# Optimization experiments

Hardware: AMD Instinct MI355X
Metric: run time of the kernel (lower is better)

Reference implementation:

```python
import jax, jax.numpy as jnp
import numpy as np
from jax import lax

K_NEIGHBORS = 15
LAM = 1.0
EPS = 1e-8


def _cdist(a):
    # Euclidean pairwise distance, safe sqrt (zero diag has zero grad path handled in bwd module too)
    sq = jnp.sum(a * a, axis=1)
    d2 = sq[:, None] + sq[None, :] - 2.0 * (a @ a.T)
    d2 = jnp.maximum(d2, 0.0)
    safe = jnp.where(d2 > 0.0, d2, 1.0)
    return jnp.where(d2 > 0.0, jnp.sqrt(safe), 0.0)


def _knn_loss(z, x, k):
    B = x.shape[0]
    x_dist = _cdist(x)
    z_dist = _cdist(z)
    eye = jnp.eye(B, dtype=bool)
    x_ns = jnp.where(eye, jnp.inf, x_dist)  # fill_diagonal_(inf)
    _, knn_idx = lax.top_k(-x_ns, k)        # k smallest per row
    mask = jnp.zeros((B, B), dtype=bool).at[jnp.arange(B)[:, None], knn_idx].set(True)
    mask = mask | mask.T
    x_max = jnp.max(jnp.where(mask, x_dist, -jnp.inf))
    z_max = jnp.max(jnp.where(mask, z_dist, -jnp.inf))
    x_norm = x_dist / (x_max + EPS)
    z_norm = z_dist / (z_max + EPS)
    diff2 = (z_norm - x_norm) ** 2
    # mean over masked entries == masked_select(...).mean()
    return jnp.sum(jnp.where(mask, diff2, 0.0)) / jnp.sum(mask).astype(diff2.dtype)


def setup_inputs() -> dict:
    key = jax.random.key(0)
    ks = jax.random.split(key, 13)
    D, H1, H2, L = 1024, 2048, 512, 64

    def lin(k, fan_in, fan_out):
        bound = 1.0 / np.sqrt(fan_in)
        kw, kb = jax.random.split(k)
        w = jax.random.uniform(kw, (fan_in, fan_out), jnp.float32, -bound, bound)
        b = jax.random.uniform(kb, (fan_out,), jnp.float32, -bound, bound)
        return w, b

    x = jax.random.normal(ks[0], (8192, D), jnp.float32)
    w_e0, b_e0 = lin(ks[1], D, H1)
    w_e1, b_e1 = lin(ks[2], H1, H2)
    w_e2, b_e2 = lin(ks[3], H2, L)
    w_d0, b_d0 = lin(ks[4], L, H2)
    w_d1, b_d1 = lin(ks[5], H2, H1)
    w_d2, b_d2 = lin(ks[6], H1, D)
    return {"x": x,
            "w_e0": w_e0, "b_e0": b_e0, "w_e1": w_e1, "b_e1": b_e1, "w_e2": w_e2, "b_e2": b_e2,
            "w_d0": w_d0, "b_d0": b_d0, "w_d1": w_d1, "b_d1": b_d1, "w_d2": w_d2, "b_d2": b_d2}


def reference(x, w_e0, b_e0, w_e1, b_e1, w_e2, b_e2, w_d0, b_d0, w_d1, b_d1, w_d2, b_d2):
    h = jax.nn.relu(x @ w_e0 + b_e0)
    h = jax.nn.relu(h @ w_e1 + b_e1)
    z = h @ w_e2 + b_e2
    h = jax.nn.relu(z @ w_d0 + b_d0)
    h = jax.nn.relu(h @ w_d1 + b_d1)
    x_rec = h @ w_d2 + b_d2
    rec_loss = jnp.mean((x_rec - x) ** 2)
    knn_loss = _knn_loss(z, x, K_NEIGHBORS)
    total = rec_loss + LAM * knn_loss
    return (total, z, rec_loss, knn_loss)
```

## Files before the change

kernel.cpp:

```cpp
#include <hip/hip_runtime.h>


typedef __attribute__((ext_vector_type(8))) short bf16x8;
typedef __attribute__((ext_vector_type(4))) float f32x4;

#define DEVINL static __device__ __forceinline__

DEVINL unsigned short f2bf(float f){
  unsigned u = __float_as_uint(f);
  u += 0x7FFFu + ((u >> 16) & 1u);
  return (unsigned short)(u >> 16);
}

DEVINL int med3i(int a, int b, int c){
  int d;
  asm("v_med3_i32 %0, %1, %2, %3" : "=v"(d) : "v"(a), "v"(b), "v"(c));
  return d;
}

DEVINL void gload16(const unsigned short* g, void* lds){
  __builtin_amdgcn_global_load_lds(
      (const __attribute__((address_space(1))) unsigned int*)g,
      (__attribute__((address_space(3))) unsigned int*)lds, 16, 0, 0);
}

DEVINL void lds_barrier(){
  asm volatile("s_waitcnt lgkmcnt(0)" ::: "memory");
  __builtin_amdgcn_s_barrier();
  asm volatile("" ::: "memory");
}

#define NLISTS 39

#define INS15(NAME, R0,R1,R2,R3,R4,R5,R6,R7,R8,R9,R10,R11,R12,R13,R14)  \
  auto NAME = [&](int v){                                               \
    if (v < R14){                                                       \
      R14 = med3i(v, R13, R14); R13 = med3i(v, R12, R13);               \
      R12 = med3i(v, R11, R12); R11 = med3i(v, R10, R11);               \
      R10 = med3i(v, R9 , R10); R9  = med3i(v, R8 , R9 );               \
      R8  = med3i(v, R7 , R8 ); R7  = med3i(v, R6 , R7 );               \
      R6  = med3i(v, R5 , R6 ); R5  = med3i(v, R4 , R5 );               \
      R4  = med3i(v, R3 , R4 ); R3  = med3i(v, R2 , R3 );               \
      R2  = med3i(v, R1 , R2 ); R1  = med3i(v, R0 , R1 );               \
      R0  = min(R0, v);                                                 \
    }                                                                   \
  }

__global__ __launch_bounds__(256) void cvtT_k(const float* __restrict__ x,
    unsigned short* __restrict__ xb, float* __restrict__ xsq,
    const float* __restrict__ w0, const float* __restrict__ w1,
    const float* __restrict__ w2, const float* __restrict__ w3,
    const float* __restrict__ w4, const float* __restrict__ w5,
    unsigned short* __restrict__ t0, unsigned short* __restrict__ t1,
    unsigned short* __restrict__ t2, unsigned short* __restrict__ t3,
    unsigned short* __restrict__ t4, unsigned short* __restrict__ t5)
{
  __shared__ float t[32][33];
  const int tid = threadIdx.x;
  if (blockIdx.x >= 2048){
    int id = blockIdx.x - 2048;
    const float* w; unsigned short* wt; int K, N, loc;
    if      (id < 2048){ w = w0; wt = t0; K = 1024; N = 2048; loc = id; }
    else if (id < 3072){ w = w1; wt = t1; K = 2048; N = 512;  loc = id - 2048; }
    else if (id < 3104){ w = w2; wt = t2; K = 512;  N = 64;   loc = id - 3072; }
    else if (id < 3136){ w = w3; wt = t3; K = 64;   N = 512;  loc = id - 3104; }
    else if (id < 4160){ w = w4; wt = t4; K = 512;  N = 2048; loc = id - 3136; }
    else               { w = w5; wt = t5; K = 2048; N = 1024; loc = id - 4160; }
    const int ntn = N >> 5;
    const int n0 = (loc % ntn) << 5, k0 = (loc / ntn) << 5;
    const int tx = tid & 31, ty = tid >> 5;
    #pragma unroll
    for (int q = 0; q < 4; q++)
      t[ty + 8*q][tx] = w[(size_t)(k0 + ty + 8*q) * N + n0 + tx];
    __syncthreads();
    #pragma unroll
    for (int q = 0; q < 4; q++)
      wt[(size_t)(n0 + ty + 8*q) * K + k0 + tx] = f2bf(t[tx][ty + 8*q]);
    return;
  }
  const int lane = tid & 63, wv = tid >> 6;
  const int row = blockIdx.x * 4 + wv;
  const float4* px = (const float4*)(x + (size_t)row * 1024);
  ushort4* pb = (ushort4*)(xb + (size_t)row * 1024);
  float ss = 0.f;
  #pragma unroll
  for (int q = 0; q < 4; q++){
    float4 v = px[q * 64 + lane];
    ss += v.x*v.x + v.y*v.y + v.z*v.z + v.w*v.w;
    ushort4 o; o.x = f2bf(v.x); o.y = f2bf(v.y); o.z = f2bf(v.z); o.w = f2bf(v.w);
    pb[q * 64 + lane] = o;
  }
  #pragma unroll
  for (int o = 32; o; o >>= 1) ss += __shfl_xor(ss, o);
  if (!lane) xsq[row] = ss;
}

__global__ __launch_bounds__(256, 2) void thr_k(
    const unsigned short* __restrict__ Xb, const float* __restrict__ xsq,
    int* __restrict__ thrI)
{
  __shared__ short As[128][32];
  __shared__ unsigned short d2s[128][130];
  const int tid = threadIdx.x, lane = tid & 63, wid = tid >> 6;
  const int wr = wid >> 1, wc = wid & 1;
  const int r16 = lane & 15, kg = lane >> 4;
  const int srow = lane >> 2, scol = (lane & 3) * 8;
  const float INF = __builtin_inff();
  const int b0 = blockIdx.x * 128;

  float xr[4][4];
  #pragma unroll
  for (int m = 0; m < 4; m++)
    #pragma unroll
    for (int r = 0; r < 4; r++)
      xr[m][r] = xsq[b0 + wr*64 + m*16 + kg*4 + r];

  const unsigned short* pa = Xb + (size_t)(b0 + wid*16 + srow) * 1024 + scol;
  short* ldsA0 = &As[wid*16][0];
  short* ldsA1 = &As[wid*16 + 64][0];

  f32x4 acc[4][4] = {};
  for (int k0 = 0; k0 < 1024; k0 += 32){
    __syncthreads();
    gload16(pa, ldsA0);
    gload16(pa + 65536, ldsA1);
    pa += 32;
    __syncthreads();
    bf16x8 af[4], bfr[4];
    #pragma unroll
    for (int m = 0; m < 4; m++) af[m]  = *(const bf16x8*)&As[wr*64 + m*16 + r16][kg*8];
    #pragma unroll
    for (int n = 0; n < 4; n++) bfr[n] = *(const bf16x8*)&As[wc*64 + n*16 + r16][kg*8];
    #pragma unroll
    for (int m = 0; m < 4; m++)
      #pragma unroll
      for (int n = 0; n < 4; n++)
        acc[m][n] = __builtin_amdgcn_mfma_f32_16x16x32_bf16(af[m], bfr[n], acc[m][n], 0, 0, 0);
  }
  float xc[4];
  #pragma unroll
  for (int n = 0; n < 4; n++) xc[n] = xsq[b0 + wc*64 + n*16 + r16];
  #pragma unroll
  for (int m = 0; m < 4; m++){
    #pragma unroll
    for (int n = 0; n < 4; n++){
      const int lc = wc*64 + n*16 + r16;
      #pragma unroll
      for (int r = 0; r < 4; r++){
        const int lr = wr*64 + m*16 + kg*4 + r;
        float v = xr[m][r] + xc[n] - 2.f * acc[m][n][r];
        if (lr == lc) v = INF;
        d2s[lr][lc] = f2bf(v);
      }
    }
  }
  __syncthreads();
  if (tid < 128){
    int r0,r1,r2,r3,r4,r5,r6,r7,r8,r9,r10,r11,r12,r13,r14;
    r0=r1=r2=r3=r4=r5=r6=r7=r8=r9=r10=r11=r12=r13=r14=0x7FFFFFFF;
    INS15(ins, r0,r1,r2,r3,r4,r5,r6,r7,r8,r9,r10,r11,r12,r13,r14);
    #pragma unroll 4
    for (int cc = 0; cc < 128; cc += 2){
      unsigned pv = *(const unsigned*)&d2s[tid][cc];
      ins((int)((pv << 16) | (unsigned)cc));
      ins((int)((pv & 0xFFFF0000u) | (unsigned)(cc + 1)));
    }
    thrI[b0 + tid] = (int)(((unsigned)r14 & 0xFFFF0000u) | 0xFFFFu);
  }
}

template<int BM, int BN, int WM, int WN, bool RELU, int OMODE>
__global__ __launch_bounds__(256, 2) void gemm_bt(
    const unsigned short* __restrict__ A, const unsigned short* __restrict__ Bt,
    const float* __restrict__ bias, int M, int N, int K,
    unsigned short* __restrict__ Cb, float* __restrict__ Cf,
    const float* __restrict__ Xref, float* __restrict__ recPart)
{
  constexpr int FM = BM / (WM * 16), FN = BN / (WN * 16);
  constexpr int AIT = (BM/16 + 3) / 4, BIT = (BN/16 + 3) / 4;
  __shared__ short As[BM][32];
  __shared__ short Bs[BN][32];
  __shared__ float wsum[4];
  const int tid = threadIdx.x, lane = tid & 63, wid = tid >> 6;
  const int wr = wid / WN, wc = wid % WN;
  const int r16 = lane & 15, kg = lane >> 4;
  const int row0 = blockIdx.x * BM, col0 = blockIdx.y * BN;
  const int srow = lane >> 2, scol = (lane & 3) * 8;
  (void)M;
  const size_t chS = (size_t)64 * K;
  const unsigned short* pa = A  + (size_t)(row0 + wid*16 + srow) * K + scol;
  const unsigned short* pb = Bt + (size_t)(col0 + wid*16 + srow) * K + scol;
  f32x4 acc[FM][FN] = {};
  for (int k0 = 0; k0 < K; k0 += 32){
    __syncthreads();
    #pragma unroll
    for (int it = 0; it < AIT; ++it)
      if (it*4 + wid < BM/16)
        gload16(pa + it*chS, &As[(it*4 + wid)*16][0]);
    #pragma unroll
    for (int it = 0; it < BIT; ++it)
      if (it*4 + wid < BN/16)
        gload16(pb + it*chS, &Bs[(it*4 + wid)*16][0]);
    pa += 32; pb += 32;
    __syncthreads();
    bf16x8 af[FM], bfr[FN];
    #pragma unroll
    for (int m = 0; m < FM; m++) af[m]  = *(const bf16x8*)&As[wr*FM*16 + m*16 + r16][kg*8];
    #pragma unroll
    for (int n = 0; n < FN; n++) bfr[n] = *(const bf16x8*)&Bs[wc*FN*16 + n*16 + r16][kg*8];
    #pragma unroll
    for (int m = 0; m < FM; m++)
      #pragma unroll
      for (int n = 0; n < FN; n++)
        acc[m][n] = __builtin_amdgcn_mfma_f32_16x16x32_bf16(af[m], bfr[n], acc[m][n], 0, 0, 0);
  }
  float lsum = 0.f;
  #pragma unroll
  for (int m = 0; m < FM; m++){
    #pragma unroll
    for (int n = 0; n < FN; n++){
      const int gc = col0 + wc*FN*16 + n*16 + r16;
      const float bv = bias[gc];
      #pragma unroll
      for (int r = 0; r < 4; r++){
        const int gr = row0 + wr*FM*16 + m*16 + kg*4 + r;
        float v = acc[m][n][r] + bv;
        if (RELU) v = fmaxf(v, 0.f);
        if (OMODE == 2){
          float d = v - Xref[(size_t)gr * N + gc];
          lsum += d * d;
        } else {
          Cb[(size_t)gr * N + gc] = f2bf(v);
          if (OMODE == 1) Cf[(size_t)gr * N + gc] = v;
        }
      }
    }
  }
  if (OMODE == 2){
    #pragma unroll
    for (int o = 32; o; o >>= 1) lsum += __shfl_xor(lsum, o);
    if (!lane) wsum[wid] = lsum;
    __syncthreads();
    if (!tid) recPart[blockIdx.y * gridDim.x + blockIdx.x] =
        wsum[0] + wsum[1] + wsum[2] + wsum[3];
  }
}

__global__ __launch_bounds__(256, 2) void gram_topk_k(
    const unsigned short* __restrict__ Xb, const float* __restrict__ xsq,
    const int* __restrict__ thrI, int* __restrict__ topP,
    const unsigned short* __restrict__ gBt, const float* __restrict__ gBias,
    unsigned short* __restrict__ gC)
{
  __shared__ short As[128][32];
  __shared__ short Bs[128][32];
  __shared__ unsigned short d2s[128][130];
  __shared__ int colL[128][15];
  __shared__ unsigned bkt[16][256];
  const int tid = threadIdx.x, lane = tid & 63, wid = tid >> 6;
  const int wr = wid >> 1, wc = wid & 1;
  const int r16 = lane & 15, kg = lane >> 4;
  const int srow = lane >> 2, scol = (lane & 3) * 8;

  short* ldsA0 = &As[wid*16][0];  short* ldsA1 = &As[wid*16 + 64][0];
  short* ldsB0 = &Bs[wid*16][0];  short* ldsB1 = &Bs[wid*16 + 64][0];
  auto stage2 = [&](const unsigned short* pa, const unsigned short* pb){
    gload16(pa,         ldsA0);
    gload16(pa + 65536, ldsA1);
    gload16(pb,         ldsB0);
    gload16(pb + 65536, ldsB1);
  };

  if (blockIdx.x >= 512){
    const int gb = blockIdx.x - 512;
    const int row0 = (gb & 63) * 128, col0 = (gb >> 6) * 128;
    const unsigned short* pa = Xb  + (size_t)(row0 + wid*16 + srow) * 1024 + scol;
    const unsigned short* pb = gBt + (size_t)(col0 + wid*16 + srow) * 1024 + scol;
    f32x4 acc[4][4] = {};
    for (int k0 = 0; k0 < 1024; k0 += 32){
      __syncthreads();
      stage2(pa, pb);
      pa += 32; pb += 32;
      __syncthreads();
      bf16x8 af[4], bfr[4];
      #pragma unroll
      for (int m = 0; m < 4; m++) af[m]  = *(const bf16x8*)&As[wr*64 + m*16 + r16][kg*8];
      #pragma unroll
      for (int n = 0; n < 4; n++) bfr[n] = *(const bf16x8*)&Bs[wc*64 + n*16 + r16][kg*8];
      #pragma unroll
      for (int m = 0; m < 4; m++)
        #pragma unroll
        for (int n = 0; n < 4; n++)
          acc[m][n] = __builtin_amdgcn_mfma_f32_16x16x32_bf16(af[m], bfr[n], acc[m][n], 0, 0, 0);
    }
    #pragma unroll
    for (int m = 0; m < 4; m++){
      #pragma unroll
      for (int n = 0; n < 4; n++){
        const int gc = col0 + wc*64 + n*16 + r16;
        const float bv = gBias[gc];
        #pragma unroll
        for (int r = 0; r < 4; r++){
          const int gr = row0 + wr*64 + m*16 + kg*4 + r;
          gC[(size_t)gr * 2048 + gc] = f2bf(fmaxf(acc[m][n][r] + bv, 0.f));
        }
      }
    }
    return;
  }

  const float INF = __builtin_inff();
  const int INFI = 0x7FFFFFFF;
  const int bi = blockIdx.x & 63;
  const int cl = blockIdx.x >> 6;
  const int row0 = bi * 128;
  const int ntt = (cl == 7) ? 5 : 4;
  const int selrow = tid & 127, half = tid >> 7, selc0 = half * 64;
  const int thrRI = thrI[row0 + selrow];

  const unsigned short* aB = Xb + (size_t)(row0 + wid*16 + srow) * 1024 + scol;

  int r0,r1,r2,r3,r4,r5,r6,r7,r8,r9,r10,r11,r12,r13,r14;
  r0=r1=r2=r3=r4=r5=r6=r7=r8=r9=r10=r11=r12=r13=r14=INFI;
  INS15(insR, r0,r1,r2,r3,r4,r5,r6,r7,r8,r9,r10,r11,r12,r13,r14);
  int c0,c1,c2,c3,c4,c5,c6,c7,c8,c9,c10,c11,c12,c13,c14;
  INS15(insC, c0,c1,c2,c3,c4,c5,c6,c7,c8,c9,c10,c11,c12,c13,c14);

  float xr[4][4];
  #pragma unroll
  for (int m = 0; m < 4; m++)
    #pragma unroll
    for (int r = 0; r < 4; r++)
      xr[m][r] = xsq[row0 + wr*64 + m*16 + kg*4 + r];

  stage2(aB, Xb + (size_t)(((bi + cl*4) & 63) * 128 + wid*16 + srow) * 1024 + scol);

  for (int tt = 0; tt < ntt; ++tt){
    const int d = cl * 4 + tt;
    const int bj = (bi + d) & 63;
    const int j0 = bj * 128;
    const unsigned short* bB  = Xb + (size_t)(j0 + wid*16 + srow) * 1024 + scol;
    const unsigned short* bBn = Xb + (size_t)(((bi + d + 1) & 63) * 128 + wid*16 + srow) * 1024 + scol;
    const unsigned short* pa = aB;
    const unsigned short* pb = bB;
    f32x4 acc[4][4] = {};
    for (int k0 = 0; k0 < 1024; k0 += 32){
      __syncthreads();
      bf16x8 af[4], bfr[4];
      #pragma unroll
      for (int m = 0; m < 4; m++) af[m]  = *(const bf16x8*)&As[wr*64 + m*16 + r16][kg*8];
      #pragma unroll
      for (int n = 0; n < 4; n++) bfr[n] = *(const bf16x8*)&Bs[wc*64 + n*16 + r16][kg*8];
      __syncthreads();
      if (k0 + 32 < 1024){ pa += 32; pb += 32; stage2(pa, pb); }
      else if (tt + 1 < ntt) stage2(aB, bBn);
      #pragma unroll
      for (int m = 0; m < 4; m++)
        #pragma unroll
        for (int n = 0; n < 4; n++)
          acc[m][n] = __builtin_amdgcn_mfma_f32_16x16x32_bf16(af[m], bfr[n], acc[m][n], 0, 0, 0);
    }
    float xc[4];
    #pragma unroll
    for (int n = 0; n < 4; n++) xc[n] = xsq[j0 + wc*64 + n*16 + r16];
    #pragma unroll
    for (int m = 0; m < 4; m++){
      #pragma unroll
      for (int n = 0; n < 4; n++){
        const int lc = wc*64 + n*16 + r16;
        #pragma unroll
        for (int r = 0; r < 4; r++){
          const int lr = wr*64 + m*16 + kg*4 + r;
          float v = xr[m][r] + xc[n] - 2.f * acc[m][n][r];
          if (row0 + lr == j0 + lc) v = INF;
          d2s[lr][lc] = f2bf(v);
        }
      }
    }
    lds_barrier();

    {
      int cnt = 0;
      const int jg0 = j0 + selc0;
      #pragma unroll 4
      for (int cc = 0; cc < 64; cc += 2){
        unsigned pv = *(const unsigned*)&d2s[selrow][selc0 + cc];
        int p0 = (int)((pv << 16) | (unsigned)(jg0 + cc));
        int p1 = (int)((pv & 0xFFFF0000u) | (unsigned)(jg0 + cc + 1));
        if (p0 <= thrRI){
          if (cnt < 16){ bkt[cnt][tid] = (unsigned)p0; ++cnt; } else insR(p0);
        }
        if (p1 <= thrRI){
          if (cnt < 16){ bkt[cnt][tid] = (unsigned)p1; ++cnt; } else insR(p1);
        }
      }
      for (int q = 0; q < cnt; ++q) insR((int)bkt[q][tid]);
    }

    const bool doCol = (d >= 1) && (d <= 31);
    if (doCol){
      c0=c1=c2=c3=c4=c5=c6=c7=c8=c9=c10=c11=c12=c13=c14=INFI;
      const int thrCI = thrI[j0 + selrow];
      const int rbase = row0 + selc0;
      int cnt = 0;
      #pragma unroll 4
      for (int rr = 0; rr < 64; ++rr){
        unsigned v = d2s[selc0 + rr][selrow];
        int pk = (int)((v << 16) | (unsigned)(rbase + rr));
        if (pk <= thrCI){
          if (cnt < 16){ bkt[cnt][tid] = (unsigned)pk; ++cnt; } else insC(pk);
        }
      }
      for (int q = 0; q < cnt; ++q) insC((int)bkt[q][tid]);
      if (half){
        colL[selrow][0]=c0;  colL[selrow][1]=c1;  colL[selrow][2]=c2;
        colL[selrow][3]=c3;  colL[selrow][4]=c4;  colL[selrow][5]=c5;
        colL[selrow][6]=c6;  colL[selrow][7]=c7;  colL[selrow][8]=c8;
        colL[selrow][9]=c9;  colL[selrow][10]=c10; colL[selrow][11]=c11;
        colL[selrow][12]=c12; colL[selrow][13]=c13; colL[selrow][14]=c14;
      }
    }
    lds_barrier();
    if (doCol && !half){
      #pragma unroll 1
      for (int q = 0; q < 15; ++q){
        int v = colL[selrow][q];
        if (v >= c14) break;
        insC(v);
      }
      int* dst = topP + ((size_t)(j0 + selrow) * NLISTS + (8 + d - 1)) * 15;
      dst[0]=c0;  dst[1]=c1;  dst[2]=c2;  dst[3]=c3;  dst[4]=c4;
      dst[5]=c5;  dst[6]=c6;  dst[7]=c7;  dst[8]=c8;  dst[9]=c9;
      dst[10]=c10; dst[11]=c11; dst[12]=c12; dst[13]=c13; dst[14]=c14;
    }
  }
  lds_barrier();
  if (half){
    colL[selrow][0]=r0;  colL[selrow][1]=r1;  colL[selrow][2]=r2;
    colL[selrow][3]=r3;  colL[selrow][4]=r4;  colL[selrow][5]=r5;
    colL[selrow][6]=r6;  colL[selrow][7]=r7;  colL[selrow][8]=r8;
    colL[selrow][9]=r9;  colL[selrow][10]=r10; colL[selrow][11]=r11;
    colL[selrow][12]=r12; colL[selrow][13]=r13; colL[selrow][14]=r14;
  }
  lds_barrier();
  if (!half){
    #pragma unroll 1
    for (int q = 0; q < 15; ++q){
      int v = colL[selrow][q];
      if (v >= r14) break;
      insR(v);
    }
    int* dst = topP + ((size_t)(row0 + selrow) * NLISTS + cl) * 15;
    dst[0]=r0;  dst[1]=r1;  dst[2]=r2;  dst[3]=r3;  dst[4]=r4;
    dst[5]=r5;  dst[6]=r6;  dst[7]=r7;  dst[8]=r8;  dst[9]=r9;
    dst[10]=r10; dst[11]=r11; dst[12]=r12; dst[13]=r13; dst[14]=r14;
  }
}

__global__ __launch_bounds__(256) void merge_topk_k(const int* __restrict__ topP,
    int* __restrict__ knn, float* __restrict__ d2k, float* __restrict__ xpart)
{
  __shared__ float wmax[4];
  const int lane = threadIdx.x & 63, wid = threadIdx.x >> 6;
  const int row = blockIdx.x * 4 + wid;
  const int* tp = topP + (size_t)row * (NLISTS * 15);
  const int INFI = 0x7FFFFFFF;
  int c0 = tp[lane];
  int c1 = tp[lane + 64];
  int c2 = tp[lane + 128];
  int c3 = tp[lane + 192];
  int c4 = tp[lane + 256];
  int c5 = tp[lane + 320];
  int c6 = tp[lane + 384];
  int c7 = tp[lane + 448];
  int c8 = tp[lane + 512];
  int c9 = (lane < 9) ? tp[lane + 576] : INFI;
  float last = 0.f;
  for (int it = 0; it < 15; ++it){
    int m = min(min(min(c0, c1), min(c2, c3)), min(min(c4, c5), min(c6, c7)));
    m = min(m, min(c8, c9));
    #pragma unroll
    for (int o = 32; o; o >>= 1) m = min(m, __shfl_xor(m, o));
    if (!lane){
      knn[row * 15 + it] = m & 0xFFFF;
      float f = __uint_as_float((unsigned)m & 0xFFFF0000u);
      d2k[row * 15 + it] = f;
      last = f;
    }
    c0 = (c0 == m) ? INFI : c0;   c1 = (c1 == m) ? INFI : c1;
    c2 = (c2 == m) ? INFI : c2;   c3 = (c3 == m) ? INFI : c3;
    c4 = (c4 == m) ? INFI : c4;   c5 = (c5 == m) ? INFI : c5;
    c6 = (c6 == m) ? INFI : c6;   c7 = (c7 == m) ? INFI : c7;
    c8 = (c8 == m) ? INFI : c8;   c9 = (c9 == m) ? INFI : c9;
  }
  if (!lane) wmax[wid] = last;
  __syncthreads();
  if (!threadIdx.x)
    xpart[blockIdx.x] = fmaxf(fmaxf(wmax[0], wmax[1]), fmaxf(wmax[2], wmax[3]));
}

__global__ __launch_bounds__(256) void pair_sums_k(
    const float* __restrict__ z, const int* __restrict__ knn,
    const float* __restrict__ d2k,
    float* __restrict__ zzP, float* __restrict__ zxP, float* __restrict__ xxP,
    float* __restrict__ zmP, float* __restrict__ cntP)
{
  __shared__ float red[4][5];
  const int lane = threadIdx.x & 63, wid = threadIdx.x >> 6;
  float szz = 0.f, szx = 0.f, sxx = 0.f, mz = 0.f, scnt = 0.f;
  for (int p = blockIdx.x * 4 + wid; p < 122880; p += gridDim.x * 4){
    const int i = p / 15;
    const int j = knn[p];
    const float dx2 = d2k[p];
    float dd = z[(size_t)i * 64 + lane] - z[(size_t)j * 64 + lane];
    float s = dd * dd;
    #pragma unroll
    for (int o = 32; o; o >>= 1) s += __shfl_xor(s, o);
    int kj = knn[j * 15 + min(lane, 14)];
    unsigned long long m2 = __ballot(lane < 15 && kj == i);
    const float w = m2 ? 1.f : 2.f;
    float dz = sqrtf(s), dx = sqrtf(dx2);
    szz += w * s;
    szx += w * dz * dx;
    sxx += w * dx2;
    scnt += w;
    mz = fmaxf(mz, dz);
  }
  if (!lane){
    red[wid][0] = szz; red[wid][1] = szx; red[wid][2] = sxx;
    red[wid][3] = mz;  red[wid][4] = scnt;
  }
  __syncthreads();
  if (!threadIdx.x){
    float a = 0.f, b = 0.f, c = 0.f, m = 0.f, n = 0.f;
    #pragma unroll
    for (int w = 0; w < 4; w++){
      a += red[w][0]; b += red[w][1]; c += red[w][2];
      m = fmaxf(m, red[w][3]); n += red[w][4];
    }
    zzP[blockIdx.x] = a; zxP[blockIdx.x] = b; xxP[blockIdx.x] = c;
    zmP[blockIdx.x] = m; cntP[blockIdx.x] = n;
  }
}

__global__ __launch_bounds__(256) void final_reduce_k(
    const float* __restrict__ recPart, const float* __restrict__ xpart,
    const float* __restrict__ zzP, const float* __restrict__ zxP,
    const float* __restrict__ xxP, const float* __restrict__ zmP,
    const float* __restrict__ cntP, float* __restrict__ out)
{
  __shared__ float rd[4][7];
  const int t = threadIdx.x, lane = t & 63, wid = t >> 6;
  float rec = 0.f, xm = 0.f, zz = 0.f, zx = 0.f, xx = 0.f, zm = 0.f, cnt = 0.f;
  for (int i = t; i < 1024; i += 256) rec += recPart[i];
  for (int i = t; i < 2048; i += 256) xm = fmaxf(xm, xpart[i]);
  for (int i = t; i < 1920; i += 256){
    zz += zzP[i]; zx += zxP[i]; xx += xxP[i]; cnt += cntP[i];
    zm = fmaxf(zm, zmP[i]);
  }
  #pragma unroll
  for (int o = 32; o; o >>= 1){
    rec += __shfl_xor(rec, o); zz += __shfl_xor(zz, o);
    zx  += __shfl_xor(zx, o);  xx += __shfl_xor(xx, o);
    cnt += __shfl_xor(cnt, o);
    xm = fmaxf(xm, __shfl_xor(xm, o));
    zm = fmaxf(zm, __shfl_xor(zm, o));
  }
  if (!lane){
    rd[wid][0]=rec; rd[wid][1]=zz; rd[wid][2]=zx; rd[wid][3]=xx;
    rd[wid][4]=xm;  rd[wid][5]=zm; rd[wid][6]=cnt;
  }
  __syncthreads();
  if (!t){
    rec = rd[0][0]+rd[1][0]+rd[2][0]+rd[3][0];
    zz  = rd[0][1]+rd[1][1]+rd[2][1]+rd[3][1];
    zx  = rd[0][2]+rd[1][2]+rd[2][2]+rd[3][2];
    xx  = rd[0][3]+rd[1][3]+rd[2][3]+rd[3][3];
    xm  = fmaxf(fmaxf(rd[0][4],rd[1][4]), fmaxf(rd[2][4],rd[3][4]));
    zm  = fmaxf(fmaxf(rd[0][5],rd[1][5]), fmaxf(rd[2][5],rd[3][5]));
    cnt = rd[0][6]+rd[1][6]+rd[2][6]+rd[3][6];
    rec *= 1.0f / (8192.0f * 1024.0f);
    float xmax = sqrtf(xm);
    float rx = 1.0f / (xmax + 1e-8f), rz = 1.0f / (zm + 1e-8f);
    float knn = (zz * rz * rz - 2.0f * zx * rz * rx + xx * rx * rx) / cnt;
    out[0] = rec + knn;
    out[1 + 8192 * 64]     = rec;
    out[1 + 8192 * 64 + 1] = knn;
  }
}

extern "C" void kernel_launch(void* const* d_in, const int* in_sizes, int n_in,
                              void* d_out, int out_size, void* d_ws, size_t ws_size,
                              hipStream_t stream)
{
  (void)in_sizes; (void)n_in; (void)out_size;
  const float* x    = (const float*)d_in[0];
  const float* w_e0 = (const float*)d_in[1];  const float* b_e0 = (const float*)d_in[2];
  const float* w_e1 = (const float*)d_in[3];  const float* b_e1 = (const float*)d_in[4];
  const float* w_e2 = (const float*)d_in[5];  const float* b_e2 = (const float*)d_in[6];
  const float* w_d0 = (const float*)d_in[7];  const float* b_d0 = (const float*)d_in[8];
  const float* w_d1 = (const float*)d_in[9];  const float* b_d1 = (const float*)d_in[10];
  const float* w_d2 = (const float*)d_in[11]; const float* b_d2 = (const float*)d_in[12];
  float* out = (float*)d_out;

  char* ws = (char*)d_ws;
  size_t off = 0;
  auto alloc = [&](size_t bytes) -> void* {
    void* p = ws + off;
    off += (bytes + 255) & ~(size_t)255;
    return p;
  };
  unsigned short* xb   = (unsigned short*)alloc(8192ull * 1024 * 2);
  unsigned short* wte0 = (unsigned short*)alloc(2048ull * 1024 * 2);
  unsigned short* wte1 = (unsigned short*)alloc(512ull  * 2048 * 2);
  unsigned short* wte2 = (unsigned short*)alloc(64ull   * 512  * 2);
  unsigned short* wtd0 = (unsigned short*)alloc(512ull  * 64   * 2);
  unsigned short* wtd1 = (unsigned short*)alloc(2048ull * 512  * 2);
  unsigned short* wtd2 = (unsigned short*)alloc(1024ull * 2048 * 2);
  unsigned short* bufA = (unsigned short*)alloc(8192ull * 2048 * 2);
  unsigned short* bufB = (unsigned short*)alloc(8192ull * 512  * 2);
  unsigned short* zb   = (unsigned short*)alloc(8192ull * 64   * 2);
  int*   topP   = (int*)  alloc(8192ull * NLISTS * 15 * 4);
  float* xsq    = (float*)alloc(8192 * 4);
  int*   thrI   = (int*)  alloc(8192 * 4);
  int*   knn    = (int*)  alloc(8192ull * 15 * 4);
  float* d2k    = (float*)alloc(8192ull * 15 * 4);
  float* xpart  = (float*)alloc(2048 * 4);
  float* zzP    = (float*)alloc(1920 * 4);
  float* zxP    = (float*)alloc(1920 * 4);
  float* xxP    = (float*)alloc(1920 * 4);
  float* zmP    = (float*)alloc(1920 * 4);
  float* cntP   = (float*)alloc(1920 * 4);
  float* recPart= (float*)alloc(1024 * 4);
  if (off > ws_size) return;

  cvtT_k<<<8256, 256, 0, stream>>>(x, xb, xsq,
      w_e0, w_e1, w_e2, w_d0, w_d1, w_d2, wte0, wte1, wte2, wtd0, wtd1, wtd2);

  thr_k<<<64, 256, 0, stream>>>(xb, xsq, thrI);

  gram_topk_k<<<1536, 256, 0, stream>>>(xb, xsq, thrI, topP, wte0, b_e0, bufA);
  merge_topk_k<<<2048, 256, 0, stream>>>(topP, knn, d2k, xpart);

  gemm_bt<128, 64,2,2,true ,0><<<dim3(64, 8), 256, 0, stream>>>(bufA, wte1, b_e1, 8192,  512, 2048, bufB, nullptr, nullptr, nullptr);
  gemm_bt< 32, 64,2,2,false,1><<<dim3(256,1), 256, 0, stream>>>(bufB, wte2, b_e2, 8192,   64,  512, zb,   out + 1, nullptr, nullptr);
  gemm_bt<128, 64,2,2,true ,0><<<dim3(64, 8), 256, 0, stream>>>(zb,   wtd0, b_d0, 8192,  512,   64, bufB, nullptr, nullptr, nullptr);
  gemm_bt<128,128,2,2,true ,0><<<dim3(64,16), 256, 0, stream>>>(bufB, wtd1, b_d1, 8192, 2048,  512, bufA, nullptr, nullptr, nullptr);
  gemm_bt< 64,128,2,2,false,2><<<dim3(128,8), 256, 0, stream>>>(bufA, wtd2, b_d2, 8192, 1024, 2048, nullptr, nullptr, x, recPart);

  pair_sums_k<<<1920, 256, 0, stream>>>(out + 1, knn, d2k, zzP, zxP, xxP, zmP, cntP);
  final_reduce_k<<<1, 256, 0, stream>>>(recPart, xpart, zzP, zxP, xxP, zmP, cntP, out);
}
```

Measured before the change: 404.2 us.

## Split gram top-k selection into two column phases to cut LDS and raise occupancy

The fused gram/top-k kernel now writes the 128x128 distance tile to LDS in two 64-column halves. Within each half, the upper 128 threads do row selection and the lower 128 do column selection, instead of every thread doing both over a full tile. This shrinks the d2s, colL and bucket buffers (bucket capacity drops from 16 to 12) and raises launch bounds to 3 blocks per CU to improve occupancy. In exchange it adds barriers per tile, serialises the epilogue into two phases, and may cause register pressure or spills under the tighter launch bound.

```diff
diff --git a/kernel.cpp b/kernel.cpp
--- a/kernel.cpp
+++ b/kernel.cpp
@@ -31,6 +31,7 @@
 }
 
 #define NLISTS 39
+#define QCAP   12
 
 #define INS15(NAME, R0,R1,R2,R3,R4,R5,R6,R7,R8,R9,R10,R11,R12,R13,R14)  \
   auto NAME = [&](int v){                                               \
@@ -246,7 +247,7 @@
   }
 }
 
-__global__ __launch_bounds__(256, 2) void gram_topk_k(
+__global__ __launch_bounds__(256, 3) void gram_topk_k(
     const unsigned short* __restrict__ Xb, const float* __restrict__ xsq,
     const int* __restrict__ thrI, int* __restrict__ topP,
     const unsigned short* __restrict__ gBt, const float* __restrict__ gBias,
@@ -254,9 +255,9 @@
 {
   __shared__ short As[128][32];
   __shared__ short Bs[128][32];
-  __shared__ unsigned short d2s[128][130];
-  __shared__ int colL[128][15];
-  __shared__ unsigned bkt[16][256];
+  __shared__ unsigned short d2s[128][66];
+  __shared__ int colL[64][15];
+  __shared__ unsigned bkt[QCAP][256];
   const int tid = threadIdx.x, lane = tid & 63, wid = tid >> 6;
   const int wr = wid >> 1, wc = wid & 1;
   const int r16 = lane & 15, kg = lane >> 4;
@@ -315,8 +316,11 @@
   const int cl = blockIdx.x >> 6;
   const int row0 = bi * 128;
   const int ntt = (cl == 7) ? 5 : 4;
-  const int selrow = tid & 127, half = tid >> 7, selc0 = half * 64;
-  const int thrRI = thrI[row0 + selrow];
+  const bool rowDuty = (tid >= 128);
+  const int myRow = tid & 127;
+  const int myCol = tid & 63;
+  const int myH   = (tid >> 6) & 1;
+  const int thrRI = thrI[row0 + myRow];
 
   const unsigned short* aB = Xb + (size_t)(row0 + wid*16 + srow) * 1024 + scol;
 
@@ -363,94 +367,82 @@
     float xc[4];
     #pragma unroll
     for (int n = 0; n < 4; n++) xc[n] = xsq[j0 + wc*64 + n*16 + r16];
-    #pragma unroll
-    for (int m = 0; m < 4; m++){
-      #pragma unroll
-      for (int n = 0; n < 4; n++){
-        const int lc = wc*64 + n*16 + r16;
+    const bool doCol = (d >= 1) && (d <= 31);
+
+    #pragma unroll 1
+    for (int ph = 0; ph < 2; ++ph){
+      if (wc == ph){
         #pragma unroll
-        for (int r = 0; r < 4; r++){
-          const int lr = wr*64 + m*16 + kg*4 + r;
-          float v = xr[m][r] + xc[n] - 2.f * acc[m][n][r];
-          if (row0 + lr == j0 + lc) v = INF;
-          d2s[lr][lc] = f2bf(v);
+        for (int m = 0; m < 4; m++){
+          #pragma unroll
+          for (int n = 0; n < 4; n++){
+            const int lc = wc*64 + n*16 + r16;
+            #pragma unroll
+            for (int r = 0; r < 4; r++){
+              const int lr = wr*64 + m*16 + kg*4 + r;
+              float v = xr[m][r] + xc[n] - 2.f * acc[m][n][r];
+              if (row0 + lr == j0 + lc) v = INF;
+              d2s[lr][lc - ph*64] = f2bf(v);
+            }
+          }
         }
       }
-    }
-    lds_barrier();
-
-    {
-      int cnt = 0;
-      const int jg0 = j0 + selc0;
-      #pragma unroll 4
-      for (int cc = 0; cc < 64; cc += 2){
-        unsigned pv = *(const unsigned*)&d2s[selrow][selc0 + cc];
-        int p0 = (int)((pv << 16) | (unsigned)(jg0 + cc));
-        int p1 = (int)((pv & 0xFFFF0000u) | (unsigned)(jg0 + cc + 1));
-        if (p0 <= thrRI){
-          if (cnt < 16){ bkt[cnt][tid] = (unsigned)p0; ++cnt; } else insR(p0);
+      lds_barrier();
+      if (rowDuty){
+        const int jg0 = j0 + ph*64;
+        int cnt = 0;
+        #pragma unroll 4
+        for (int cc = 0; cc < 64; cc += 2){
+          unsigned pv = *(const unsigned*)&d2s[myRow][cc];
+          int p0 = (int)((pv << 16) | (unsigned)(jg0 + cc));
+          int p1 = (int)((pv & 0xFFFF0000u) | (unsigned)(jg0 + cc + 1));
+          if (p0 <= thrRI){
+            if (cnt < QCAP){ bkt[cnt][tid] = (unsigned)p0; ++cnt; } else insR(p0);
+          }
+          if (p1 <= thrRI){
+            if (cnt < QCAP){ bkt[cnt][tid] = (unsigned)p1; ++cnt; } else insR(p1);
+          }
         }
-        if (p1 <= thrRI){
-          if (cnt < 16){ bkt[cnt][tid] = (unsigned)p1; ++cnt; } else insR(p1);
+        for (int q = 0; q < cnt; ++q) insR((int)bkt[q][tid]);
+      } else if (doCol){
+        c0=c1=c2=c3=c4=c5=c6=c7=c8=c9=c10=c11=c12=c13=c14=INFI;
+        const int thrCI = thrI[j0 + ph*64 + myCol];
+        const int rbase = row0 + myH*64;
+        int cnt = 0;
+        #pragma unroll 4
+        for (int rr = 0; rr < 64; ++rr){
+          unsigned v = d2s[myH*64 + rr][myCol];
+          int pk = (int)((v << 16) | (unsigned)(rbase + rr));
+          if (pk <= thrCI){
+            if (cnt < QCAP){ bkt[cnt][tid] = (unsigned)pk; ++cnt; } else insC(pk);
+          }
+        }
+        for (int q = 0; q < cnt; ++q) insC((int)bkt[q][tid]);
+        if (myH){
+          colL[myCol][0]=c0;  colL[myCol][1]=c1;  colL[myCol][2]=c2;
+          colL[myCol][3]=c3;  colL[myCol][4]=c4;  colL[myCol][5]=c5;
+          colL[myCol][6]=c6;  colL[myCol][7]=c7;  colL[myCol][8]=c8;
+          colL[myCol][9]=c9;  colL[myCol][10]=c10; colL[myCol][11]=c11;
+          colL[myCol][12]=c12; colL[myCol][13]=c13; colL[myCol][14]=c14;
         }
       }
-      for (int q = 0; q < cnt; ++q) insR((int)bkt[q][tid]);
-    }
-
-    const bool doCol = (d >= 1) && (d <= 31);
-    if (doCol){
-      c0=c1=c2=c3=c4=c5=c6=c7=c8=c9=c10=c11=c12=c13=c14=INFI;
-      const int thrCI = thrI[j0 + selrow];
-      const int rbase = row0 + selc0;
-      int cnt = 0;
-      #pragma unroll 4
-      for (int rr = 0; rr < 64; ++rr){
-        unsigned v = d2s[selc0 + rr][selrow];
-        int pk = (int)((v << 16) | (unsigned)(rbase + rr));
-        if (pk <= thrCI){
-          if (cnt < 16){ bkt[cnt][tid] = (unsigned)pk; ++cnt; } else insC(pk);
+      lds_barrier();
+      if (doCol && tid < 64){
+        #pragma unroll 1
+        for (int q = 0; q < 15; ++q){
+          int v = colL[myCol][q];
+          if (v >= c14) break;
+          insC(v);
         }
+        int* dst = topP + ((size_t)(j0 + ph*64 + myCol) * NLISTS + (8 + d - 1)) * 15;
+        dst[0]=c0;  dst[1]=c1;  dst[2]=c2;  dst[3]=c3;  dst[4]=c4;
+        dst[5]=c5;  dst[6]=c6;  dst[7]=c7;  dst[8]=c8;  dst[9]=c9;
+        dst[10]=c10; dst[11]=c11; dst[12]=c12; dst[13]=c13; dst[14]=c14;
       }
-      for (int q = 0; q < cnt; ++q) insC((int)bkt[q][tid]);
-      if (half){
-        colL[selrow][0]=c0;  colL[selrow][1]=c1;  colL[selrow][2]=c2;
-        colL[selrow][3]=c3;  colL[selrow][4]=c4;  colL[selrow][5]=c5;
-        colL[selrow][6]=c6;  colL[selrow][7]=c7;  colL[selrow][8]=c8;
-        colL[selrow][9]=c9;  colL[selrow][10]=c10; colL[selrow][11]=c11;
-        colL[selrow][12]=c12; colL[selrow][13]=c13; colL[selrow][14]=c14;
-      }
-    }
-    lds_barrier();
-    if (doCol && !half){
-      #pragma unroll 1
-      for (int q = 0; q < 15; ++q){
-        int v = colL[selrow][q];
-        if (v >= c14) break;
-        insC(v);
-      }
-      int* dst = topP + ((size_t)(j0 + selrow) * NLISTS + (8 + d - 1)) * 15;
-      dst[0]=c0;  dst[1]=c1;  dst[2]=c2;  dst[3]=c3;  dst[4]=c4;
-      dst[5]=c5;  dst[6]=c6;  dst[7]=c7;  dst[8]=c8;  dst[9]=c9;
-      dst[10]=c10; dst[11]=c11; dst[12]=c12; dst[13]=c13; dst[14]=c14;
-    }
-  }
-  lds_barrier();
-  if (half){
-    colL[selrow][0]=r0;  colL[selrow][1]=r1;  colL[selrow][2]=r2;
-    colL[selrow][3]=r3;  colL[selrow][4]=r4;  colL[selrow][5]=r5;
-    colL[selrow][6]=r6;  colL[selrow][7]=r7;  colL[selrow][8]=r8;
-    colL[selrow][9]=r9;  colL[selrow][10]=r10; colL[selrow][11]=r11;
-    colL[selrow][12]=r12; colL[selrow][13]=r13; colL[selrow][14]=r14;
-  }
-  lds_barrier();
-  if (!half){
-    #pragma unroll 1
-    for (int q = 0; q < 15; ++q){
-      int v = colL[selrow][q];
-      if (v >= r14) break;
-      insR(v);
-    }
-    int* dst = topP + ((size_t)(row0 + selrow) * NLISTS + cl) * 15;
+    }
+  }
+  if (rowDuty){
+    int* dst = topP + ((size_t)(row0 + myRow) * NLISTS + cl) * 15;
     dst[0]=r0;  dst[1]=r1;  dst[2]=r2;  dst[3]=r3;  dst[4]=r4;
     dst[5]=r5;  dst[6]=r6;  dst[7]=r7;  dst[8]=r8;  dst[9]=r9;
     dst[10]=r10; dst[11]=r11; dst[12]=r12; dst[13]=r13; dst[14]=r14;
```

Result: slower. 427.7 us (+5.8%).
